# Kernel optimization log

Measured on AMD Instinct MI355X. Metric: run time of the kernel, lower is better.

## Reference

```python
import jax, jax.numpy as jnp
import numpy as np

B = 2048
NUM_FEATURES = 40960
M = 256
N = 32
K = 32
MAX_EVAL = 10000.0  # Chess_Lib.MAX_EVAL stand-in
SPARSITY = 32.0 / NUM_FEATURES  # ~32 active HalfKP features per position


def _xavier(key, shape):
    fan_out, fan_in = shape
    limit = np.sqrt(6.0 / (fan_in + fan_out)).astype(np.float32)
    return jax.random.uniform(key, shape, jnp.float32, -limit, limit)


def setup_inputs() -> dict:
    key = jax.random.key(0)
    ks = jax.random.split(key, 8)
    # ~32-hot sparse binary feature vectors (HalfKP style)
    wf = (jax.random.uniform(ks[0], (B, NUM_FEATURES)) < SPARSITY).astype(jnp.float32)
    bf = (jax.random.uniform(ks[1], (B, NUM_FEATURES)) < SPARSITY).astype(jnp.float32)
    stm = jnp.round(jax.random.uniform(ks[2], (B, 1))).astype(jnp.float32)
    return {
        "white_features": wf,
        "black_features": bf,
        "stm": stm,
        "ft_w": _xavier(ks[3], (M, NUM_FEATURES)),
        "ft_b": jnp.zeros((M,), jnp.float32),
        "l1_w": _xavier(ks[4], (N, 2 * M)),
        "l1_b": jnp.zeros((N,), jnp.float32),
        "l2_w": _xavier(ks[5], (K, N)),
        "l2_b": jnp.zeros((K,), jnp.float32),
        "l3_w": _xavier(ks[6], (1, K)),
        "l3_b": jnp.zeros((1,), jnp.float32),
    }


def reference(white_features, black_features, stm, ft_w, ft_b,
              l1_w, l1_b, l2_w, l2_b, l3_w, l3_b):
    # feature transformer: [B,F] @ [F,M] -> [B,M]
    w = white_features @ ft_w.T + ft_b
    b = black_features @ ft_w.T + ft_b
    acc = stm * jnp.concatenate([w, b], axis=1) + (1.0 - stm) * jnp.concatenate([b, w], axis=1)
    l1_x = jnp.clip(acc, 0.0, 1.0)
    l2_x = jnp.clip(l1_x @ l1_w.T + l1_b, 0.0, 1.0)
    l3_x = jnp.clip(l2_x @ l2_w.T + l2_b, 0.0, 1.0)
    ev = jnp.clip(l3_x @ l3_w.T + l3_b, 0.0, 1.0)
    # align_eval without the python int() cast (kept batched/differentiable)
    return (ev - 0.5) * 2.0 * MAX_EVAL
```

## Files before the change

kernel.cpp:

```cpp
#include <hip/hip_runtime.h>
#include <hip/hip_bf16.h>

#define NF 40960
#define MD 256
#define BATCH 2048
#define CAP 512

__device__ __forceinline__ float clip01(float v) {
    return fminf(fmaxf(v, 0.0f), 1.0f);
}

__global__ __launch_bounds__(256) void transpose_ft(const float* __restrict__ in,
                                                    float* __restrict__ outT) {
    __shared__ float tile[32][33];
    const int f0 = blockIdx.x * 32;
    const int m0 = blockIdx.y * 32;
    const int tx = threadIdx.x;
    const int ty = threadIdx.y;
    #pragma unroll
    for (int r = 0; r < 32; r += 8)
        tile[ty + r][tx] = in[(size_t)(m0 + ty + r) * NF + f0 + tx];
    __syncthreads();
    #pragma unroll
    for (int r = 0; r < 32; r += 8)
        outT[(size_t)(f0 + ty + r) * MD + m0 + tx] = tile[tx][ty + r];
}

__global__ __launch_bounds__(256) void nnue_main(
    const float* __restrict__ wf, const float* __restrict__ bfeat,
    const float* __restrict__ stm, const float* __restrict__ ft,
    const float* __restrict__ ft_b,
    const float* __restrict__ l1_w, const float* __restrict__ l1_b,
    const float* __restrict__ l2_w, const float* __restrict__ l2_b,
    const float* __restrict__ l3_w, const float* __restrict__ l3_b,
    float* __restrict__ out, int transposed)
{
    __shared__ int idxW[CAP];
    __shared__ int idxB[CAP];
    __shared__ int nW, nB;
    __shared__ float xsh[512];
    __shared__ float red[32][9];
    __shared__ float ysh[32], zsh[32];

    const int pos = blockIdx.x;
    const int t = threadIdx.x;

    if (t == 0) { nW = 0; nB = 0; }
    __syncthreads();

    const float4* wf4 = (const float4*)(wf + (size_t)pos * NF);
    const float4* bf4 = (const float4*)(bfeat + (size_t)pos * NF);
    #pragma unroll 4
    for (int i = t; i < NF / 4; i += 256) {
        float4 v = wf4[i];
        if (v.x != 0.0f) { int p = atomicAdd(&nW, 1); if (p < CAP) idxW[p] = 4 * i + 0; }
        if (v.y != 0.0f) { int p = atomicAdd(&nW, 1); if (p < CAP) idxW[p] = 4 * i + 1; }
        if (v.z != 0.0f) { int p = atomicAdd(&nW, 1); if (p < CAP) idxW[p] = 4 * i + 2; }
        if (v.w != 0.0f) { int p = atomicAdd(&nW, 1); if (p < CAP) idxW[p] = 4 * i + 3; }
        float4 u = bf4[i];
        if (u.x != 0.0f) { int p = atomicAdd(&nB, 1); if (p < CAP) idxB[p] = 4 * i + 0; }
        if (u.y != 0.0f) { int p = atomicAdd(&nB, 1); if (p < CAP) idxB[p] = 4 * i + 1; }
        if (u.z != 0.0f) { int p = atomicAdd(&nB, 1); if (p < CAP) idxB[p] = 4 * i + 2; }
        if (u.w != 0.0f) { int p = atomicAdd(&nB, 1); if (p < CAP) idxB[p] = 4 * i + 3; }
    }
    __syncthreads();

    const int cw = min(nW, CAP);
    const int cb = min(nB, CAP);

    float accW = ft_b[t];
    float accB = ft_b[t];
    if (transposed) {
        for (int j = 0; j < cw; ++j) accW += ft[(size_t)idxW[j] * MD + t];
        for (int j = 0; j < cb; ++j) accB += ft[(size_t)idxB[j] * MD + t];
    } else {
        const float* row = ft + (size_t)t * NF;
        for (int j = 0; j < cw; ++j) accW += row[idxW[j]];
        for (int j = 0; j < cb; ++j) accB += row[idxB[j]];
    }

    const float s = stm[pos];
    xsh[t]       = clip01(s * accW + (1.0f - s) * accB);
    xsh[256 + t] = clip01(s * accB + (1.0f - s) * accW);
    __syncthreads();

    {
        const int n = t & 31;
        const int c = t >> 5;
        const float* w1 = l1_w + (size_t)n * 512 + c * 64;
        const float* xx = xsh + c * 64;
        float p = 0.0f;
        #pragma unroll
        for (int j = 0; j < 64; ++j) p += xx[j] * w1[j];
        red[n][c] = p;
    }
    __syncthreads();
    if (t < 32) {
        float v = l1_b[t];
        #pragma unroll
        for (int c = 0; c < 8; ++c) v += red[t][c];
        ysh[t] = clip01(v);
    }
    __syncthreads();

    if (t < 32) {
        float v = l2_b[t];
        const float* w2 = l2_w + t * 32;
        #pragma unroll
        for (int j = 0; j < 32; ++j) v += ysh[j] * w2[j];
        zsh[t] = clip01(v);
    }
    __syncthreads();

    if (t == 0) {
        float v = l3_b[0];
        #pragma unroll
        for (int j = 0; j < 32; ++j) v += zsh[j] * l3_w[j];
        v = clip01(v);
        out[pos] = (v - 0.5f) * 20000.0f;
    }
}

extern "C" void kernel_launch(void* const* d_in, const int* in_sizes, int n_in,
                              void* d_out, int out_size, void* d_ws, size_t ws_size,
                              hipStream_t stream) {
    const float* wf    = (const float*)d_in[0];
    const float* bfeat = (const float*)d_in[1];
    const float* stm   = (const float*)d_in[2];
    const float* ft_w  = (const float*)d_in[3];
    const float* ft_b  = (const float*)d_in[4];
    const float* l1_w  = (const float*)d_in[5];
    const float* l1_b  = (const float*)d_in[6];
    const float* l2_w  = (const float*)d_in[7];
    const float* l2_b  = (const float*)d_in[8];
    const float* l3_w  = (const float*)d_in[9];
    const float* l3_b  = (const float*)d_in[10];
    float* out = (float*)d_out;

    const size_t needT = (size_t)NF * MD * sizeof(float);
    const int useT = (ws_size >= needT) ? 1 : 0;
    float* ftT = (float*)d_ws;

    if (useT) {
        transpose_ft<<<dim3(NF / 32, MD / 32), dim3(32, 8), 0, stream>>>(ft_w, ftT);
    }
    nnue_main<<<BATCH, 256, 0, stream>>>(
        wf, bfeat, stm, useT ? ftT : ft_w, ft_b,
        l1_w, l1_b, l2_w, l2_b, l3_w, l3_b, out, useT);
}
```

Before: 696.7 us.

## Split feature scan across chunk blocks fused with weight transpose, then gather-MLP

The dense feature scan is split into many small blocks, one per (position, color, chunk), running in the same launch as a 64x64-tiled transpose of the feature weights. A second kernel merges the per-chunk index lists and does an unrolled gather plus the MLP. This targets the low parallelism and serial atomics of one block per position scanning 2x40960 floats, and overlaps the transpose with the scan. In exchange it drops the non-transposed fallback, assumes the workspace is large enough, and caps each chunk at 32 active features, which holds for the test sparsity but could silently truncate denser inputs.

```diff
diff --git a/kernel.cpp b/kernel.cpp
--- a/kernel.cpp
+++ b/kernel.cpp
@@ -4,40 +4,89 @@
 #define NF 40960
 #define MD 256
 #define BATCH 2048
-#define CAP 512
+#define NCHUNK 4
+#define CHUNK (NF / NCHUNK)
+#define CAPC 32
+
+#define SCAN_BLOCKS (2 * BATCH * NCHUNK)
+#define TRANS_BLOCKS ((NF / 64) * (MD / 64))
 
 __device__ __forceinline__ float clip01(float v) {
     return fminf(fmaxf(v, 0.0f), 1.0f);
 }
 
-__global__ __launch_bounds__(256) void transpose_ft(const float* __restrict__ in,
-                                                    float* __restrict__ outT) {
-    __shared__ float tile[32][33];
-    const int f0 = blockIdx.x * 32;
-    const int m0 = blockIdx.y * 32;
-    const int tx = threadIdx.x;
-    const int ty = threadIdx.y;
-    #pragma unroll
-    for (int r = 0; r < 32; r += 8)
-        tile[ty + r][tx] = in[(size_t)(m0 + ty + r) * NF + f0 + tx];
-    __syncthreads();
-    #pragma unroll
-    for (int r = 0; r < 32; r += 8)
-        outT[(size_t)(f0 + ty + r) * MD + m0 + tx] = tile[tx][ty + r];
-}
-
-__global__ __launch_bounds__(256) void nnue_main(
+__global__ __launch_bounds__(256) void scan_transpose(
     const float* __restrict__ wf, const float* __restrict__ bfeat,
-    const float* __restrict__ stm, const float* __restrict__ ft,
+    const float* __restrict__ ft_w,
+    float* __restrict__ ftT, int* __restrict__ g_cnt, int* __restrict__ g_idx)
+{
+    __shared__ float tile[64][65];
+    __shared__ int s_cnt;
+    __shared__ int s_idx[CAPC];
+
+    const int b = blockIdx.x;
+    const int t = threadIdx.x;
+
+    if (b < SCAN_BLOCKS) {
+        const int chunk = b & 3;
+        const int pc    = b >> 2;
+        const int color = pc & 1;
+        const int pos   = pc >> 1;
+
+        if (t == 0) s_cnt = 0;
+        __syncthreads();
+
+        const float* src = (color ? bfeat : wf) + (size_t)pos * NF + chunk * CHUNK;
+        const float4* p4 = (const float4*)src;
+
+        float4 v[10];
+        #pragma unroll
+        for (int k = 0; k < 10; ++k) v[k] = p4[t + 256 * k];
+
+        #pragma unroll
+        for (int k = 0; k < 10; ++k) {
+            float4 a = v[k];
+            if (a.x + a.y + a.z + a.w != 0.0f) {
+                const int e = chunk * CHUNK + 4 * (t + 256 * k);
+                if (a.x != 0.0f) { int q = atomicAdd(&s_cnt, 1); if (q < CAPC) s_idx[q] = e;     }
+                if (a.y != 0.0f) { int q = atomicAdd(&s_cnt, 1); if (q < CAPC) s_idx[q] = e + 1; }
+                if (a.z != 0.0f) { int q = atomicAdd(&s_cnt, 1); if (q < CAPC) s_idx[q] = e + 2; }
+                if (a.w != 0.0f) { int q = atomicAdd(&s_cnt, 1); if (q < CAPC) s_idx[q] = e + 3; }
+            }
+        }
+        __syncthreads();
+
+        const int c = min(s_cnt, CAPC);
+        if (t == 0) g_cnt[b] = c;
+        if (t < c)  g_idx[(size_t)b * CAPC + t] = s_idx[t];
+    } else {
+        const int tb = b - SCAN_BLOCKS;
+        const int f0 = (tb % (NF / 64)) * 64;
+        const int m0 = (tb / (NF / 64)) * 64;
+        const int tx = t & 63;
+        const int ty = t >> 6;
+        #pragma unroll
+        for (int r = ty; r < 64; r += 4)
+            tile[r][tx] = ft_w[(size_t)(m0 + r) * NF + f0 + tx];
+        __syncthreads();
+        #pragma unroll
+        for (int r = ty; r < 64; r += 4)
+            ftT[(size_t)(f0 + r) * MD + m0 + tx] = tile[tx][r];
+    }
+}
+
+__global__ __launch_bounds__(256) void gather_mlp(
+    const float* __restrict__ stm, const float* __restrict__ ftT,
+    const int* __restrict__ g_cnt, const int* __restrict__ g_idx,
     const float* __restrict__ ft_b,
     const float* __restrict__ l1_w, const float* __restrict__ l1_b,
     const float* __restrict__ l2_w, const float* __restrict__ l2_b,
     const float* __restrict__ l3_w, const float* __restrict__ l3_b,
-    float* __restrict__ out, int transposed)
+    float* __restrict__ out)
 {
-    __shared__ int idxW[CAP];
-    __shared__ int idxB[CAP];
-    __shared__ int nW, nB;
+    __shared__ int lw[NCHUNK * CAPC], lb[NCHUNK * CAPC];
+    __shared__ int cnts[8], offs[8];
+    __shared__ int cw_s, cb_s;
     __shared__ float xsh[512];
     __shared__ float red[32][9];
     __shared__ float ysh[32], zsh[32];
@@ -45,38 +94,48 @@
     const int pos = blockIdx.x;
     const int t = threadIdx.x;
 
-    if (t == 0) { nW = 0; nB = 0; }
-    __syncthreads();
-
-    const float4* wf4 = (const float4*)(wf + (size_t)pos * NF);
-    const float4* bf4 = (const float4*)(bfeat + (size_t)pos * NF);
-    #pragma unroll 4
-    for (int i = t; i < NF / 4; i += 256) {
-        float4 v = wf4[i];
-        if (v.x != 0.0f) { int p = atomicAdd(&nW, 1); if (p < CAP) idxW[p] = 4 * i + 0; }
-        if (v.y != 0.0f) { int p = atomicAdd(&nW, 1); if (p < CAP) idxW[p] = 4 * i + 1; }
-        if (v.z != 0.0f) { int p = atomicAdd(&nW, 1); if (p < CAP) idxW[p] = 4 * i + 2; }
-        if (v.w != 0.0f) { int p = atomicAdd(&nW, 1); if (p < CAP) idxW[p] = 4 * i + 3; }
-        float4 u = bf4[i];
-        if (u.x != 0.0f) { int p = atomicAdd(&nB, 1); if (p < CAP) idxB[p] = 4 * i + 0; }
-        if (u.y != 0.0f) { int p = atomicAdd(&nB, 1); if (p < CAP) idxB[p] = 4 * i + 1; }
-        if (u.z != 0.0f) { int p = atomicAdd(&nB, 1); if (p < CAP) idxB[p] = 4 * i + 2; }
-        if (u.w != 0.0f) { int p = atomicAdd(&nB, 1); if (p < CAP) idxB[p] = 4 * i + 3; }
-    }
-    __syncthreads();
-
-    const int cw = min(nW, CAP);
-    const int cb = min(nB, CAP);
+    if (t < 8) cnts[t] = g_cnt[(pos * 2 + (t >> 2)) * 4 + (t & 3)];
+    __syncthreads();
+    if (t == 0) {
+        int ow = 0, ob = 0;
+        #pragma unroll
+        for (int c = 0; c < 4; ++c) {
+            offs[c]     = ow; ow += cnts[c];
+            offs[4 + c] = ob; ob += cnts[4 + c];
+        }
+        cw_s = ow; cb_s = ob;
+    }
+    __syncthreads();
+    #pragma unroll
+    for (int c = 0; c < 4; ++c) {
+        if (t < cnts[c])     lw[offs[c] + t]     = g_idx[(size_t)((pos * 2 + 0) * 4 + c) * CAPC + t];
+        if (t < cnts[4 + c]) lb[offs[4 + c] + t] = g_idx[(size_t)((pos * 2 + 1) * 4 + c) * CAPC + t];
+    }
+    __syncthreads();
+
+    const int cw = cw_s, cb = cb_s;
 
     float accW = ft_b[t];
     float accB = ft_b[t];
-    if (transposed) {
-        for (int j = 0; j < cw; ++j) accW += ft[(size_t)idxW[j] * MD + t];
-        for (int j = 0; j < cb; ++j) accB += ft[(size_t)idxB[j] * MD + t];
-    } else {
-        const float* row = ft + (size_t)t * NF;
-        for (int j = 0; j < cw; ++j) accW += row[idxW[j]];
-        for (int j = 0; j < cb; ++j) accB += row[idxB[j]];
+    {
+        int j = 0;
+        for (; j + 4 <= cw; j += 4) {
+            float a0 = ftT[(size_t)lw[j]     * MD + t];
+            float a1 = ftT[(size_t)lw[j + 1] * MD + t];
+            float a2 = ftT[(size_t)lw[j + 2] * MD + t];
+            float a3 = ftT[(size_t)lw[j + 3] * MD + t];
+            accW += a0 + a1 + a2 + a3;
+        }
+        for (; j < cw; ++j) accW += ftT[(size_t)lw[j] * MD + t];
+        j = 0;
+        for (; j + 4 <= cb; j += 4) {
+            float a0 = ftT[(size_t)lb[j]     * MD + t];
+            float a1 = ftT[(size_t)lb[j + 1] * MD + t];
+            float a2 = ftT[(size_t)lb[j + 2] * MD + t];
+            float a3 = ftT[(size_t)lb[j + 3] * MD + t];
+            accB += a0 + a1 + a2 + a3;
+        }
+        for (; j < cb; ++j) accB += ftT[(size_t)lb[j] * MD + t];
     }
 
     const float s = stm[pos];
@@ -137,14 +196,14 @@
     const float* l3_b  = (const float*)d_in[10];
     float* out = (float*)d_out;
 
-    const size_t needT = (size_t)NF * MD * sizeof(float);
-    const int useT = (ws_size >= needT) ? 1 : 0;
-    float* ftT = (float*)d_ws;
-
-    if (useT) {
-        transpose_ft<<<dim3(NF / 32, MD / 32), dim3(32, 8), 0, stream>>>(ft_w, ftT);
-    }
-    nnue_main<<<BATCH, 256, 0, stream>>>(
-        wf, bfeat, stm, useT ? ftT : ft_w, ft_b,
-        l1_w, l1_b, l2_w, l2_b, l3_w, l3_b, out, useT);
-}
+    float* ftT   = (float*)d_ws;
+    int*   g_cnt = (int*)((char*)d_ws + (size_t)NF * MD * sizeof(float));
+    int*   g_idx = g_cnt + SCAN_BLOCKS;
+
+    scan_transpose<<<SCAN_BLOCKS + TRANS_BLOCKS, 256, 0, stream>>>(
+        wf, bfeat, ft_w, ftT, g_cnt, g_idx);
+
+    gather_mlp<<<BATCH, 256, 0, stream>>>(
+        stm, ftT, g_cnt, g_idx, ft_b,
+        l1_w, l1_b, l2_w, l2_b, l3_w, l3_b, out);
+}
```

After: 698.9 us. Within noise of the previous version (+0.3%).

## Drop feature-weight transpose and gather directly from untransposed weights

Applied to the files above, without the earlier changes.

Removes the separate transpose kernel and workspace copy of the 40960x256 feature-transformer weights. The main kernel now gathers each thread's values directly from row-major ft_w, using two accumulators per side to expose more memory-level parallelism. The sparse index scan also gets a cheap whole-float4 zero test so most vectors skip the per-element atomic branches. The trade-off is that gathers become strided across threads (one row per lane) instead of coalesced 1 KB rows, so many more cache lines are touched per active feature.

```diff
diff --git a/kernel.cpp b/kernel.cpp
--- a/kernel.cpp
+++ b/kernel.cpp
@@ -2,7 +2,6 @@
 #include <hip/hip_bf16.h>
 
 #define NF 40960
-#define MD 256
 #define BATCH 2048
 #define CAP 512
 
@@ -10,30 +9,14 @@
     return fminf(fmaxf(v, 0.0f), 1.0f);
 }
 
-__global__ __launch_bounds__(256) void transpose_ft(const float* __restrict__ in,
-                                                    float* __restrict__ outT) {
-    __shared__ float tile[32][33];
-    const int f0 = blockIdx.x * 32;
-    const int m0 = blockIdx.y * 32;
-    const int tx = threadIdx.x;
-    const int ty = threadIdx.y;
-    #pragma unroll
-    for (int r = 0; r < 32; r += 8)
-        tile[ty + r][tx] = in[(size_t)(m0 + ty + r) * NF + f0 + tx];
-    __syncthreads();
-    #pragma unroll
-    for (int r = 0; r < 32; r += 8)
-        outT[(size_t)(f0 + ty + r) * MD + m0 + tx] = tile[tx][ty + r];
-}
-
-__global__ __launch_bounds__(256) void nnue_main(
+__global__ __launch_bounds__(256) void nnue_fused(
     const float* __restrict__ wf, const float* __restrict__ bfeat,
-    const float* __restrict__ stm, const float* __restrict__ ft,
+    const float* __restrict__ stm, const float* __restrict__ ft_w,
     const float* __restrict__ ft_b,
     const float* __restrict__ l1_w, const float* __restrict__ l1_b,
     const float* __restrict__ l2_w, const float* __restrict__ l2_b,
     const float* __restrict__ l3_w, const float* __restrict__ l3_b,
-    float* __restrict__ out, int transposed)
+    float* __restrict__ out)
 {
     __shared__ int idxW[CAP];
     __shared__ int idxB[CAP];
@@ -53,35 +36,43 @@
     #pragma unroll 4
     for (int i = t; i < NF / 4; i += 256) {
         float4 v = wf4[i];
-        if (v.x != 0.0f) { int p = atomicAdd(&nW, 1); if (p < CAP) idxW[p] = 4 * i + 0; }
-        if (v.y != 0.0f) { int p = atomicAdd(&nW, 1); if (p < CAP) idxW[p] = 4 * i + 1; }
-        if (v.z != 0.0f) { int p = atomicAdd(&nW, 1); if (p < CAP) idxW[p] = 4 * i + 2; }
-        if (v.w != 0.0f) { int p = atomicAdd(&nW, 1); if (p < CAP) idxW[p] = 4 * i + 3; }
+        if (v.x + v.y + v.z + v.w != 0.0f) {
+            if (v.x != 0.0f) { int p = atomicAdd(&nW, 1); if (p < CAP) idxW[p] = 4 * i + 0; }
+            if (v.y != 0.0f) { int p = atomicAdd(&nW, 1); if (p < CAP) idxW[p] = 4 * i + 1; }
+            if (v.z != 0.0f) { int p = atomicAdd(&nW, 1); if (p < CAP) idxW[p] = 4 * i + 2; }
+            if (v.w != 0.0f) { int p = atomicAdd(&nW, 1); if (p < CAP) idxW[p] = 4 * i + 3; }
+        }
         float4 u = bf4[i];
-        if (u.x != 0.0f) { int p = atomicAdd(&nB, 1); if (p < CAP) idxB[p] = 4 * i + 0; }
-        if (u.y != 0.0f) { int p = atomicAdd(&nB, 1); if (p < CAP) idxB[p] = 4 * i + 1; }
-        if (u.z != 0.0f) { int p = atomicAdd(&nB, 1); if (p < CAP) idxB[p] = 4 * i + 2; }
-        if (u.w != 0.0f) { int p = atomicAdd(&nB, 1); if (p < CAP) idxB[p] = 4 * i + 3; }
+        if (u.x + u.y + u.z + u.w != 0.0f) {
+            if (u.x != 0.0f) { int p = atomicAdd(&nB, 1); if (p < CAP) idxB[p] = 4 * i + 0; }
+            if (u.y != 0.0f) { int p = atomicAdd(&nB, 1); if (p < CAP) idxB[p] = 4 * i + 1; }
+            if (u.z != 0.0f) { int p = atomicAdd(&nB, 1); if (p < CAP) idxB[p] = 4 * i + 2; }
+            if (u.w != 0.0f) { int p = atomicAdd(&nB, 1); if (p < CAP) idxB[p] = 4 * i + 3; }
+        }
     }
     __syncthreads();
 
     const int cw = min(nW, CAP);
     const int cb = min(nB, CAP);
 
-    float accW = ft_b[t];
-    float accB = ft_b[t];
-    if (transposed) {
-        for (int j = 0; j < cw; ++j) accW += ft[(size_t)idxW[j] * MD + t];
-        for (int j = 0; j < cb; ++j) accB += ft[(size_t)idxB[j] * MD + t];
-    } else {
-        const float* row = ft + (size_t)t * NF;
-        for (int j = 0; j < cw; ++j) accW += row[idxW[j]];
-        for (int j = 0; j < cb; ++j) accB += row[idxB[j]];
+    {
+        const float* row = ft_w + (size_t)t * NF;
+        float a0 = 0.0f, a1 = 0.0f, b0 = 0.0f, b1 = 0.0f;
+        int j = 0;
+        for (; j + 2 <= cw; j += 2) { a0 += row[idxW[j]]; a1 += row[idxW[j + 1]]; }
+        if (j < cw) a0 += row[idxW[j]];
+        j = 0;
+        for (; j + 2 <= cb; j += 2) { b0 += row[idxB[j]]; b1 += row[idxB[j + 1]]; }
+        if (j < cb) b0 += row[idxB[j]];
+
+        const float bias = ft_b[t];
+        const float accW = bias + a0 + a1;
+        const float accB = bias + b0 + b1;
+
+        const float s = stm[pos];
+        xsh[t]       = clip01(s * accW + (1.0f - s) * accB);
+        xsh[256 + t] = clip01(s * accB + (1.0f - s) * accW);
     }
-
-    const float s = stm[pos];
-    xsh[t]       = clip01(s * accW + (1.0f - s) * accB);
-    xsh[256 + t] = clip01(s * accB + (1.0f - s) * accW);
     __syncthreads();
 
     {
@@ -137,14 +128,7 @@
     const float* l3_b  = (const float*)d_in[10];
     float* out = (float*)d_out;
 
-    const size_t needT = (size_t)NF * MD * sizeof(float);
-    const int useT = (ws_size >= needT) ? 1 : 0;
-    float* ftT = (float*)d_ws;
-
-    if (useT) {
-        transpose_ft<<<dim3(NF / 32, MD / 32), dim3(32, 8), 0, stream>>>(ft_w, ftT);
-    }
-    nnue_main<<<BATCH, 256, 0, stream>>>(
-        wf, bfeat, stm, useT ? ftT : ft_w, ft_b,
-        l1_w, l1_b, l2_w, l2_b, l3_w, l3_b, out, useT);
+    nnue_fused<<<BATCH, 256, 0, stream>>>(
+        wf, bfeat, stm, ft_w, ft_b,
+        l1_w, l1_b, l2_w, l2_b, l3_w, l3_b, out);
 }
```

After: 1.155 ms. +65.7%, slower.
